# Optimization experiments

Hardware: AMD Instinct MI355X
Metric: run time of the kernel (lower is better)

The kernel has to match this reference:

```python
import jax, jax.numpy as jnp
import numpy as np

V, E, H = 32000, 256, 512
B, S, T = 32, 80, 80


def setup_inputs() -> dict:
    key = jax.random.key(0)
    ks = jax.random.split(key, 16)
    s = 0.05
    emb = jax.random.normal(ks[0], (V, E), jnp.float32) * s
    emb = emb.at[0].set(0.0)  # padding_idx=0 row is zero
    inp = {
        "src": jax.random.randint(ks[1], (B, S), 0, V),
        "tgt": jax.random.randint(ks[2], (B, T), 0, V),
        "emb": emb,
        "enc_Wih": jax.random.normal(ks[3], (3 * H, E), jnp.float32) * s,
        "enc_Whh": jax.random.normal(ks[4], (3 * H, H), jnp.float32) * s,
        "enc_bih": jax.random.normal(ks[5], (3 * H,), jnp.float32) * s,
        "enc_bhh": jax.random.normal(ks[6], (3 * H,), jnp.float32) * s,
        "dec_Wih": jax.random.normal(ks[7], (3 * H, E), jnp.float32) * s,
        "dec_Whh": jax.random.normal(ks[8], (3 * H, H), jnp.float32) * s,
        "dec_bih": jax.random.normal(ks[9], (3 * H,), jnp.float32) * s,
        "dec_bhh": jax.random.normal(ks[10], (3 * H,), jnp.float32) * s,
        "out_W": jax.random.normal(ks[11], (V, 2 * H), jnp.float32) * s,
        "out_b": jax.random.normal(ks[12], (V,), jnp.float32) * s,
    }
    return inp


def _gru_cell(x, h, Wih, Whh, bih, bhh):
    # PyTorch GRU cell: gates ordered (r, z, n)
    gi = x @ Wih.T + bih          # (B, 3H)
    gh = h @ Whh.T + bhh          # (B, 3H)
    i_r, i_z, i_n = jnp.split(gi, 3, axis=-1)
    h_r, h_z, h_n = jnp.split(gh, 3, axis=-1)
    r = jax.nn.sigmoid(i_r + h_r)
    z = jax.nn.sigmoid(i_z + h_z)
    n = jnp.tanh(i_n + r * h_n)
    return (1.0 - z) * n + z * h


def reference(src, tgt, emb, enc_Wih, enc_Whh, enc_bih, enc_bhh,
              dec_Wih, dec_Whh, dec_bih, dec_bhh, out_W, out_b):
    Bsz, Tlen = tgt.shape

    # ---- encoder: single-layer GRU over src ----
    x_src = emb[src]                              # (B, S, E)
    h0 = jnp.zeros((Bsz, H), x_src.dtype)

    def enc_step(h, x_t):
        h = _gru_cell(x_t, h, enc_Wih, enc_Whh, enc_bih, enc_bhh)
        return h, h

    h_enc, enc_outs = jax.lax.scan(enc_step, h0, jnp.swapaxes(x_src, 0, 1))
    enc_outs = jnp.swapaxes(enc_outs, 0, 1)       # (B, S, H)

    # ---- decoder: teacher forcing (ratio=1.0), steps t=1..T-1 ----
    x_dec = emb[tgt[:, :-1]]                      # (B, T-1, E)

    def dec_step(h, x_t):
        h = _gru_cell(x_t, h, dec_Wih, dec_Whh, dec_bih, dec_bhh)
        # Luong dot attention on new hidden state
        scores = jnp.einsum('bsh,bh->bs', enc_outs, h)
        aw = jax.nn.softmax(scores, axis=1)
        ctx = jnp.einsum('bs,bsh->bh', aw, enc_outs)
        combined = jnp.concatenate([h, ctx], axis=1)   # (B, 2H)
        step_logits = combined @ out_W.T + out_b       # (B, V)
        return h, step_logits

    _, step_logits = jax.lax.scan(dec_step, h_enc, jnp.swapaxes(x_dec, 0, 1))
    step_logits = jnp.swapaxes(step_logits, 0, 1)      # (B, T-1, V)

    # logits[:, 0, :] stays zero, matching the torch module
    logits = jnp.concatenate(
        [jnp.zeros((Bsz, 1, V), step_logits.dtype), step_logits], axis=1)
    return logits
```

## Files before the change

kernel.cpp:

```cpp
#include <hip/hip_runtime.h>

#define VV 32000
#define EE 256
#define HH 512
#define BB 32
#define SS 80
#define TT 80

typedef __attribute__((ext_vector_type(8))) _Float16 half8;
typedef __attribute__((ext_vector_type(4))) _Float16 half4;
typedef __attribute__((ext_vector_type(4))) float floatx4;
typedef unsigned long long u64;

__device__ __forceinline__ void gload16(const _Float16* g, _Float16* l) {
  __builtin_amdgcn_global_load_lds((const __attribute__((address_space(1))) void*)g,
                                   (__attribute__((address_space(3))) void*)l, 16, 0, 0);
}

__device__ __forceinline__ u64 aload(const u64* p) {
  return __hip_atomic_load(p, __ATOMIC_RELAXED, __HIP_MEMORY_SCOPE_AGENT);
}
__device__ __forceinline__ void astore(u64* p, u64 v) {
  __hip_atomic_store(p, v, __ATOMIC_RELAXED, __HIP_MEMORY_SCOPE_AGENT);
}

__device__ __forceinline__ unsigned pack15(unsigned short u) {
  return (u & 0x3FFFu) | ((u >> 1) & 0x4000u);
}
__device__ __forceinline__ unsigned short unpack15(unsigned v) {
  return (unsigned short)((v & 0x3FFFu) | ((v & 0x4000u) << 1));
}
__device__ __forceinline__ u64 unpack_word4(u64 a) {
  u64 o = 0;
#pragma unroll
  for (int i = 0; i < 4; ++i)
    o |= (u64)unpack15((unsigned)(a >> (15*i)) & 0x7FFFu) << (16*i);
  return o;
}

__device__ __forceinline__ float dot8(half8 a, half8 b, float c) {
  typedef __attribute__((ext_vector_type(2))) _Float16 half2v;
  half2v a0 = {a[0],a[1]}, a1 = {a[2],a[3]}, a2 = {a[4],a[5]}, a3 = {a[6],a[7]};
  half2v b0 = {b[0],b[1]}, b1 = {b[2],b[3]}, b2 = {b[4],b[5]}, b3 = {b[6],b[7]};
  c = __builtin_amdgcn_fdot2(a0, b0, c, false);
  c = __builtin_amdgcn_fdot2(a1, b1, c, false);
  c = __builtin_amdgcn_fdot2(a2, b2, c, false);
  c = __builtin_amdgcn_fdot2(a3, b3, c, false);
  return c;
}

__device__ __forceinline__ float sigm(float x) { return 1.f/(1.f + __expf(-x)); }
__device__ __forceinline__ float tanh_f(float x) { return 2.f/(1.f + __expf(-2.f*x)) - 1.f; }

__global__ __launch_bounds__(256) void prep_all(
    const int* __restrict__ src, const int* __restrict__ tgt,
    const float* __restrict__ emb,
    const float* __restrict__ eWih, const float* __restrict__ ebih,
    const float* __restrict__ dWih, const float* __restrict__ dbih,
    const float* __restrict__ outW, _Float16* __restrict__ oWh,
    float* __restrict__ giE, float* __restrict__ giD)
{
  const int pblk = blockIdx.x;
  const int tid = threadIdx.x;

  if (pblk >= 480) {
    const int pid = pblk - 480;
    const long total8 = (long)VV*1024/8;
    for (long i = (long)pid*256 + tid; i < total8; i += 512L*256) {
      const float* s_ = outW + i*8;
      const floatx4 a = *(const floatx4*)s_;
      const floatx4 b = *(const floatx4*)(s_ + 4);
      half8 h;
      h[0]=(_Float16)a[0]; h[1]=(_Float16)a[1]; h[2]=(_Float16)a[2]; h[3]=(_Float16)a[3];
      h[4]=(_Float16)b[0]; h[5]=(_Float16)b[1]; h[6]=(_Float16)b[2]; h[7]=(_Float16)b[3];
      *(half8*)(oWh + i*8) = h;
    }
    return;
  }

  __shared__ _Float16 As[4096];
  __shared__ _Float16 Bs[4096];
  const int lane = tid & 63;
  const int wv = tid >> 6;
  const int wr = wv >> 1, wc = wv & 1;
  const int mt = pblk / 24;
  const int ntx = pblk % 24;
  const bool isE = ntx < 12;
  const int nt = isE ? ntx : ntx - 12;
  const float* Wih = isE ? eWih : dWih;
  const float* bih = isE ? ebih : dbih;
  float* gi = isE ? giE : giD;
  floatx4 acc[4][4];
#pragma unroll
  for (int i=0;i<4;++i)
#pragma unroll
    for (int j=0;j<4;++j) acc[i][j] = (floatx4){0.f,0.f,0.f,0.f};
  const int r2 = tid >> 1, cb = (tid & 1) * 16;
  const int R = mt*128 + r2;
  int tok = -1;
  if (isE) tok = src[R];
  else if (R < 2528) { const int b_ = R/79, tt = R - b_*79; tok = tgt[b_*80 + tt]; }
  const float* arow = (tok >= 0) ? emb + (size_t)tok*EE : nullptr;
  const float* brow = Wih + (size_t)(nt*128 + r2)*EE;
  const int g8 = (lane >> 4) * 8;
  const int lr = lane & 15;
  for (int kb = 0; kb < EE; kb += 32) {
    __syncthreads();
    if (arow) {
#pragma unroll
      for (int q = 0; q < 4; ++q) {
        const floatx4 va = *(const floatx4*)(arow + kb + cb + q*4);
#pragma unroll
        for (int e = 0; e < 4; ++e) As[r2*32 + cb + q*4 + e] = (_Float16)va[e];
      }
    } else {
#pragma unroll
      for (int q = 0; q < 16; ++q) As[r2*32 + cb + q] = (_Float16)0.f;
    }
#pragma unroll
    for (int q = 0; q < 4; ++q) {
      const floatx4 vb = *(const floatx4*)(brow + kb + cb + q*4);
#pragma unroll
      for (int e = 0; e < 4; ++e) Bs[r2*32 + cb + q*4 + e] = (_Float16)vb[e];
    }
    __syncthreads();
    half8 af[4], bf[4];
#pragma unroll
    for (int i=0;i<4;++i) af[i] = *(const half8*)(As + (wr*64 + i*16 + lr)*32 + g8);
#pragma unroll
    for (int j=0;j<4;++j) bf[j] = *(const half8*)(Bs + (wc*64 + j*16 + lr)*32 + g8);
#pragma unroll
    for (int i=0;i<4;++i)
#pragma unroll
      for (int j=0;j<4;++j)
        acc[i][j] = __builtin_amdgcn_mfma_f32_16x16x32_f16(af[i], bf[j], acc[i][j], 0,0,0);
  }
  const int rm = 4*(lane>>4);
#pragma unroll
  for (int i=0;i<4;++i)
#pragma unroll
    for (int r=0;r<4;++r) {
      const int row = mt*128 + wr*64 + i*16 + rm + r;
      if (isE || row < 2528) {
#pragma unroll
        for (int j=0;j<4;++j) {
          const int col = nt*128 + wc*64 + j*16 + lr;
          gi[(size_t)row*1536 + col] = acc[i][j][r] + bih[col];
        }
      }
    }
}

__global__ __launch_bounds__(256) void logits_gemm(
    const _Float16* __restrict__ A, const _Float16* __restrict__ Bm,
    const float* __restrict__ bias, float* __restrict__ out)
{
  const int p = blockIdx.x;
  const int x = p & 7, s = p >> 3;
  const int nt = x + 8*(s / 20);
  const int mt = s % 20;
  if (nt >= 250) return;
  __shared__ _Float16 As[4096];
  __shared__ _Float16 Bs[4096];
  const int tid = threadIdx.x;
  const int lane = tid & 63;
  const int wv = tid >> 6;
  const int wr = wv >> 1, wc = wv & 1;
  floatx4 acc[4][4];
#pragma unroll
  for (int i=0;i<4;++i)
#pragma unroll
    for (int j=0;j<4;++j) acc[i][j] = (floatx4){0.f,0.f,0.f,0.f};
  const int srow = lane >> 2;
  const int scol = (lane & 3) * 8;
  const _Float16* Ab = A + (size_t)(mt*128)*1024;
  const _Float16* Bb = Bm + (size_t)(nt*128)*1024;
  const int g8 = (lane >> 4) * 8;
  const int lr = lane & 15;
  for (int kb = 0; kb < 1024; kb += 32) {
    __syncthreads();
#pragma unroll
    for (int cc = 0; cc < 2; ++cc) {
      const int c = wv*2 + cc;
      gload16(Ab + (size_t)(c*16 + srow)*1024 + kb + scol, As + c*512);
      gload16(Bb + (size_t)(c*16 + srow)*1024 + kb + scol, Bs + c*512);
    }
    __syncthreads();
    half8 af[4], bf[4];
#pragma unroll
    for (int i=0;i<4;++i) af[i] = *(const half8*)(As + (wr*64 + i*16 + lr)*32 + g8);
#pragma unroll
    for (int j=0;j<4;++j) bf[j] = *(const half8*)(Bs + (wc*64 + j*16 + lr)*32 + g8);
#pragma unroll
    for (int i=0;i<4;++i)
#pragma unroll
      for (int j=0;j<4;++j)
        acc[i][j] = __builtin_amdgcn_mfma_f32_16x16x32_f16(af[i], bf[j], acc[i][j], 0,0,0);
  }
  const int rm = 4*(lane>>4);
#pragma unroll
  for (int i=0;i<4;++i)
#pragma unroll
    for (int r=0;r<4;++r) {
      const int row = mt*128 + wr*64 + i*16 + rm + r;
#pragma unroll
      for (int j=0;j<4;++j) {
        const int col = nt*128 + wc*64 + j*16 + lr;
        if (row < 2528) {
          const int b = row / 79;
          const int t = row - b*79;
          out[(size_t)(b*80 + t + 1)*VV + col] = acc[i][j][r] + bias[col];
        } else {
          out[(size_t)((row - 2528)*80)*VV + col] = 0.f;
        }
      }
    }
}

#define SEQ_SMEM (80*512*2 + 512*2 + 512*2 + 3*64*8*4 + 2*80*4)
__global__ __launch_bounds__(512) void seq_pb(
    const float* __restrict__ eWhh, const float* __restrict__ dWhh,
    const float* __restrict__ ebhh, const float* __restrict__ dbhh,
    const float* __restrict__ giE, const float* __restrict__ giD,
    u64* __restrict__ hx,
    _Float16* __restrict__ comb)
{
  extern __shared__ char smem[];
  _Float16* eo_l = (_Float16*)smem;
  _Float16* hbuf = eo_l + 80*512;
  _Float16* hatt = hbuf + 512;
  float* part = (float*)(hatt + 512);
  float* sc = part + 3*64*8;
  float* aw = sc + 80;

  const int bi = blockIdx.x;
  const int q = bi >> 5, b = bi & 31;
  const int tid = threadIdx.x;
  const int lane = tid & 63;
  const int wv = tid >> 6;
  const int jl = tid & 63;
  const int kq = tid >> 6;
  const int j  = q*64 + jl;

  half8 wreg[3][8];
  auto loadW = [&](const float* W){
#pragma unroll
    for (int g = 0; g < 3; ++g)
#pragma unroll
      for (int c = 0; c < 8; ++c) {
        const float* s8 = W + ((size_t)(g*512 + j))*512 + kq*64 + c*8;
        const floatx4 a = *(const floatx4*)s8;
        const floatx4 d = *(const floatx4*)(s8 + 4);
        half8 h;
        h[0]=(_Float16)a[0]; h[1]=(_Float16)a[1]; h[2]=(_Float16)a[2]; h[3]=(_Float16)a[3];
        h[4]=(_Float16)d[0]; h[5]=(_Float16)d[1]; h[6]=(_Float16)d[2]; h[7]=(_Float16)d[3];
        wreg[g][c] = h;
      }
  };

  auto consume = [&](int slotR, u64 rtag){
    if (tid < 112) {
      const int m = tid + (tid >= q*16 ? 16 : 0);
      const u64* sp = hx + (size_t)slotR*4096 + b*128 + m;
      u64 v = aload(sp);
      int guard = 0;
      while ((v >> 60) != rtag && guard < (1<<22)) { v = aload(sp); ++guard; }
      *(u64*)&hbuf[m*4] = unpack_word4(v);
    }
    __syncthreads();
  };
  auto publish = [&](int slotW, u64 wtag){
    if (tid < 16) {
      const int m = q*16 + tid;
      u64 wq = wtag << 60;
#pragma unroll
      for (int e = 0; e < 4; ++e) {
        union { _Float16 h; unsigned short u; } cv; cv.h = hbuf[m*4 + e];
        wq |= (u64)pack15(cv.u) << (15*e);
      }
      astore(hx + (size_t)slotW*4096 + b*128 + m, wq);
    }
  };

  float hp = 0.f;
  auto gru = [&](float gr_, float gz_, float gn_, float bR, float bZ, float bN){
    half8 hv[8];
#pragma unroll
    for (int c = 0; c < 8; ++c) hv[c] = *(const half8*)&hbuf[kq*64 + c*8];
    float p0 = 0.f, p1 = 0.f, p2 = 0.f;
#pragma unroll
    for (int c = 0; c < 8; ++c) {
      p0 = dot8(wreg[0][c], hv[c], p0);
      p1 = dot8(wreg[1][c], hv[c], p1);
      p2 = dot8(wreg[2][c], hv[c], p2);
    }
    part[(0*64 + jl)*8 + kq] = p0;
    part[(1*64 + jl)*8 + kq] = p1;
    part[(2*64 + jl)*8 + kq] = p2;
    __syncthreads();
    if (tid < 64) {
      float a0 = 0.f, a1 = 0.f, a2 = 0.f;
#pragma unroll
      for (int e = 0; e < 8; ++e) {
        a0 += part[(0*64 + tid)*8 + e];
        a1 += part[(1*64 + tid)*8 + e];
        a2 += part[(2*64 + tid)*8 + e];
      }
      const float rg = sigm(gr_ + a0 + bR);
      const float zg = sigm(gz_ + a1 + bZ);
      const float ng = tanh_f(gn_ + rg*(a2 + bN));
      const float hn = (1.f - zg)*ng + zg*hp;
      hp = hn;
      hbuf[q*64 + tid] = (_Float16)hn;
    }
    __syncthreads();
  };

  auto attention = [&](int trow){
    const half8 hf = *(const half8*)&hatt[lane*8];
#pragma unroll 2
    for (int i = 0; i < 10; ++i) {
      const int s = wv*10 + i;
      const half8 ev = *(const half8*)&eo_l[s*512 + lane*8];
      float pt = dot8(ev, hf, 0.f);
#pragma unroll
      for (int o = 32; o; o >>= 1) pt += __shfl_xor(pt, o);
      if (lane == 0) sc[s] = pt;
    }
    __syncthreads();
    if (wv == 0) {
      const float v0 = sc[lane];
      const float v1 = (lane < 16) ? sc[64+lane] : -1e30f;
      float m = fmaxf(v0, v1);
#pragma unroll
      for (int o = 32; o; o >>= 1) m = fmaxf(m, __shfl_xor(m, o));
      const float e0 = __expf(v0 - m);
      const float e1 = (lane < 16) ? __expf(v1 - m) : 0.f;
      float ssum = e0 + e1;
#pragma unroll
      for (int o = 32; o; o >>= 1) ssum += __shfl_xor(ssum, o);
      const float inv = 1.f/ssum;
      aw[lane] = e0*inv;
      if (lane < 16) aw[64+lane] = e1*inv;
    }
    __syncthreads();
    if (tid < 64) {
      float c = 0.f;
#pragma unroll 8
      for (int s = 0; s < SS; ++s) c += aw[s] * (float)eo_l[s*512 + q*64 + tid];
      _Float16* cr = comb + ((size_t)b*79 + trow)*1024;
      cr[q*64 + tid]       = hatt[q*64 + tid];
      cr[512 + q*64 + tid] = (_Float16)c;
    }
    __syncthreads();
  };

  if (tid < 128) *(u64*)&hbuf[tid*4] = 0ull;
  loadW(eWhh);
  float ebR=0.f, ebZ=0.f, ebN=0.f, dbR=0.f, dbZ=0.f, dbN=0.f;
  if (tid < 64) {
    ebR = ebhh[j]; ebZ = ebhh[512+j]; ebN = ebhh[1024+j];
    dbR = dbhh[j]; dbZ = dbhh[512+j]; dbN = dbhh[1024+j];
  }
  __syncthreads();

  for (int k = 0; k < SS; ++k) {
    float gr_=0.f, gz_=0.f, gn_=0.f;
    if (tid < 64) {
      const float* gi = giE + ((size_t)b*SS + k)*1536;
      gr_ = gi[j]; gz_ = gi[512+j]; gn_ = gi[1024+j];
    }
    consume(k & 1, (u64)(k & 15));
    if (k > 0 && tid < 128)
      *(u64*)&eo_l[(k-1)*512 + tid*4] = *(const u64*)&hbuf[tid*4];
    gru(gr_, gz_, gn_, ebR, ebZ, ebN);
    publish((k+1) & 1, (u64)((k+1) & 15));
  }

  loadW(dWhh);

  for (int t = 0; t < TT-1; ++t) {
    const int k = 80 + t;
    float gr_=0.f, gz_=0.f, gn_=0.f;
    if (tid < 64) {
      const float* gi = giD + ((size_t)b*79 + t)*1536;
      gr_ = gi[j]; gz_ = gi[512+j]; gn_ = gi[1024+j];
    }
    consume(k & 1, (u64)(k & 15));
    if (tid < 128) {
      if (t == 0) *(u64*)&eo_l[79*512 + tid*4] = *(const u64*)&hbuf[tid*4];
      else        *(u64*)&hatt[tid*4]          = *(const u64*)&hbuf[tid*4];
    }
    gru(gr_, gz_, gn_, dbR, dbZ, dbN);
    publish((k+1) & 1, (u64)((k+1) & 15));
    if (t > 0) attention(t-1);
  }

  if (tid < 112) {
    const int m = tid + (tid >= q*16 ? 16 : 0);
    const u64* sp = hx + (size_t)4096 + b*128 + m;
    u64 v = aload(sp);
    int guard = 0;
    while ((v >> 60) != 15ull && guard < (1<<22)) { v = aload(sp); ++guard; }
    *(u64*)&hbuf[m*4] = unpack_word4(v);
  }
  __syncthreads();
  if (tid < 128) *(u64*)&hatt[tid*4] = *(const u64*)&hbuf[tid*4];
  __syncthreads();
  attention(TT-2);
}

extern "C" void kernel_launch(void* const* d_in, const int* in_sizes, int n_in,
                              void* d_out, int out_size, void* d_ws, size_t ws_size,
                              hipStream_t stream) {
  (void)in_sizes; (void)n_in; (void)out_size; (void)ws_size;
  const int*   src  = (const int*)d_in[0];
  const int*   tgt  = (const int*)d_in[1];
  const float* emb  = (const float*)d_in[2];
  const float* eWih = (const float*)d_in[3];
  const float* eWhh = (const float*)d_in[4];
  const float* ebih = (const float*)d_in[5];
  const float* ebhh = (const float*)d_in[6];
  const float* dWih = (const float*)d_in[7];
  const float* dWhh = (const float*)d_in[8];
  const float* dbih = (const float*)d_in[9];
  const float* dbhh = (const float*)d_in[10];
  const float* outW = (const float*)d_in[11];
  const float* outb = (const float*)d_in[12];
  float* out = (float*)d_out;

  char* p = (char*)d_ws;
  auto alloc = [&](size_t n){ char* r = p; p += (n + 255) & ~(size_t)255; return r; };
  _Float16* oWh  = (_Float16*)alloc((size_t)VV*1024*2);
  float*    giE  = (float*)alloc((size_t)2560*1536*4);
  float*    giD  = (float*)alloc((size_t)2560*1536*4);
  u64*      hx   = (u64*)alloc((size_t)2*32*128*8);
  _Float16* comb = (_Float16*)alloc((size_t)2560*1024*2);

  hipMemsetAsync(hx, 0, (size_t)2*32*128*8, stream);
  prep_all<<<992, 256, 0, stream>>>(src, tgt, emb, eWih, ebih, dWih, dbih,
                                    outW, oWh, giE, giD);
  hipFuncSetAttribute((const void*)seq_pb,
                      hipFuncAttributeMaxDynamicSharedMemorySize, SEQ_SMEM);
  seq_pb<<<256, 512, SEQ_SMEM, stream>>>(eWhh, dWhh, ebhh, dbhh, giE, giD,
                                         hx, comb);
  logits_gemm<<<5120, 256, 0, stream>>>(comb, oWh, outb, out);
}
```

Before: 967.6 us.

## Use sc0 inline-asm polling for cross-block handoff and fold memset into prep

Replaces the relaxed atomic spin loop in the recurrent hidden-state exchange with an inline-asm global load carrying the sc0 cache bit. It tries that path for a bounded number of iterations, then falls back to the atomic loop. Publish now does a volatile store followed by the atomic store. The hx zeroing moves from a separate hipMemsetAsync into four extra blocks of the prep kernel, saving one launch. The goal is lower per-step handoff latency in the persistent sequential kernel, at the risk of subtle cache-coherence issues and a duplicate store.

```diff
diff --git a/kernel.cpp b/kernel.cpp
--- a/kernel.cpp
+++ b/kernel.cpp
@@ -22,6 +22,12 @@
 }
 __device__ __forceinline__ void astore(u64* p, u64 v) {
   __hip_atomic_store(p, v, __ATOMIC_RELAXED, __HIP_MEMORY_SCOPE_AGENT);
+}
+__device__ __forceinline__ u64 ld_sc0(const u64* p) {
+  u64 v;
+  asm volatile("global_load_dwordx2 %0, %1, off sc0\n\ts_waitcnt vmcnt(0)"
+               : "=v"(v) : "v"(p) : "memory");
+  return v;
 }
 
 __device__ __forceinline__ unsigned pack15(unsigned short u) {
@@ -58,11 +64,17 @@
     const float* __restrict__ eWih, const float* __restrict__ ebih,
     const float* __restrict__ dWih, const float* __restrict__ dbih,
     const float* __restrict__ outW, _Float16* __restrict__ oWh,
-    float* __restrict__ giE, float* __restrict__ giD)
+    float* __restrict__ giE, float* __restrict__ giD,
+    u64* __restrict__ hx)
 {
   const int pblk = blockIdx.x;
   const int tid = threadIdx.x;
 
+  if (pblk >= 992) {
+    const int pid = pblk - 992;
+    for (int i = pid*256 + tid; i < 8192; i += 4*256) astore(hx + i, 0ull);
+    return;
+  }
   if (pblk >= 480) {
     const int pid = pblk - 480;
     const long total8 = (long)VV*1024/8;
@@ -262,9 +274,18 @@
     if (tid < 112) {
       const int m = tid + (tid >= q*16 ? 16 : 0);
       const u64* sp = hx + (size_t)slotR*4096 + b*128 + m;
-      u64 v = aload(sp);
-      int guard = 0;
-      while ((v >> 60) != rtag && guard < (1<<22)) { v = aload(sp); ++guard; }
+      u64 v;
+      int fast = 64;
+      for (;;) {
+        v = ld_sc0(sp);
+        if ((v >> 60) == rtag) break;
+        if (--fast == 0) {
+          v = aload(sp);
+          int guard = 0;
+          while ((v >> 60) != rtag && guard < (1<<22)) { v = aload(sp); ++guard; }
+          break;
+        }
+      }
       *(u64*)&hbuf[m*4] = unpack_word4(v);
     }
     __syncthreads();
@@ -278,7 +299,9 @@
         union { _Float16 h; unsigned short u; } cv; cv.h = hbuf[m*4 + e];
         wq |= (u64)pack15(cv.u) << (15*e);
       }
-      astore(hx + (size_t)slotW*4096 + b*128 + m, wq);
+      u64* gp = hx + (size_t)slotW*4096 + b*128 + m;
+      *(volatile u64*)gp = wq;
+      astore(gp, wq);
     }
   };
 
@@ -399,9 +422,18 @@
   if (tid < 112) {
     const int m = tid + (tid >= q*16 ? 16 : 0);
     const u64* sp = hx + (size_t)4096 + b*128 + m;
-    u64 v = aload(sp);
-    int guard = 0;
-    while ((v >> 60) != 15ull && guard < (1<<22)) { v = aload(sp); ++guard; }
+    u64 v;
+    int fast = 64;
+    for (;;) {
+      v = ld_sc0(sp);
+      if ((v >> 60) == 15ull) break;
+      if (--fast == 0) {
+        v = aload(sp);
+        int guard = 0;
+        while ((v >> 60) != 15ull && guard < (1<<22)) { v = aload(sp); ++guard; }
+        break;
+      }
+    }
     *(u64*)&hbuf[m*4] = unpack_word4(v);
   }
   __syncthreads();
@@ -437,9 +469,8 @@
   u64*      hx   = (u64*)alloc((size_t)2*32*128*8);
   _Float16* comb = (_Float16*)alloc((size_t)2560*1024*2);
 
-  hipMemsetAsync(hx, 0, (size_t)2*32*128*8, stream);
-  prep_all<<<992, 256, 0, stream>>>(src, tgt, emb, eWih, ebih, dWih, dbih,
-                                    outW, oWh, giE, giD);
+  prep_all<<<996, 256, 0, stream>>>(src, tgt, emb, eWih, ebih, dWih, dbih,
+                                    outW, oWh, giE, giD, hx);
   hipFuncSetAttribute((const void*)seq_pb,
                       hipFuncAttributeMaxDynamicSharedMemorySize, SEQ_SMEM);
   seq_pb<<<256, 512, SEQ_SMEM, stream>>>(eWhh, dWhh, ebhh, dbhh, giE, giD,
```

Result: slower. 1.727 ms (+78.4%).
